# Optimization experiments

Hardware: AMD Instinct MI355X
Metric: run time of the kernel (lower is better)

The kernel has to match this reference:

```python
import jax
import jax.numpy as jnp
from jax import lax
import numpy as np

B, C, Hsp, Wsp = 16, 256, 64, 64
E, HID = 4, 128          # num_experts, expert_hidden
RH = 128                 # router_hidden
TOP_K = 1
EPS = 1e-9


def setup_inputs() -> dict:
    key = jax.random.key(0)
    ks = jax.random.split(key, 8)
    s = lambda *shape: 1.0 / np.sqrt(shape[-1])
    x = jax.random.normal(ks[0], (B, C, Hsp, Wsp), dtype=jnp.float32)
    # router: Linear(C->RH), Linear(RH->E)
    Wr1 = jax.random.normal(ks[1], (RH, C), dtype=jnp.float32) * s(RH, C)
    br1 = jnp.zeros((RH,), dtype=jnp.float32)
    Wr2 = jax.random.normal(ks[2], (E, RH), dtype=jnp.float32) * s(E, RH)
    br2 = jnp.zeros((E,), dtype=jnp.float32)
    # experts (stacked over E): 1x1 C->HID, 3x3 HID->HID, 1x1 HID->C, all bias-free
    W1 = jax.random.normal(ks[3], (E, HID, C), dtype=jnp.float32) * s(E, HID, C)
    W2 = jax.random.normal(ks[4], (E, HID, HID, 3, 3), dtype=jnp.float32) * (1.0 / np.sqrt(HID * 9))
    W3 = jax.random.normal(ks[5], (E, C, HID), dtype=jnp.float32) * s(E, C, HID)
    return {"x": x, "Wr1": Wr1, "br1": br1, "Wr2": Wr2, "br2": br2,
            "W1": W1, "W2": W2, "W3": W3}


def reference(x, Wr1, br1, Wr2, br2, W1, W2, W3):
    b = x.shape[0]
    # --- router on globally pooled features ---
    pooled = x.mean(axis=(2, 3))                      # [B, C]
    h = jax.nn.relu(pooled @ Wr1.T + br1)             # [B, RH]
    logits = h @ Wr2.T + br2                          # [B, E]
    probs = jax.nn.softmax(logits, axis=1)
    # top-k masking + renormalize (top_k < num_experts)
    vals, idx = lax.top_k(probs, TOP_K)               # [B, k]
    mask = jnp.zeros_like(probs).at[jnp.arange(b)[:, None], idx].set(vals)
    probs = mask / (mask.sum(axis=1, keepdims=True) + EPS)
    # --- run all experts (as in original) ---
    # 1x1 conv C->HID, per expert:  [B, E, HID, H, W]
    y1 = jax.nn.relu(jnp.einsum('bcij,ehc->behij', x, W1))
    # 3x3 grouped conv (one group per expert), HID->HID
    y1m = y1.reshape(b, E * HID, Hsp, Wsp)
    y2 = lax.conv_general_dilated(
        y1m, W2.reshape(E * HID, HID, 3, 3),
        window_strides=(1, 1), padding='SAME',
        feature_group_count=E,
        dimension_numbers=('NCHW', 'OIHW', 'NCHW'))
    y2 = jax.nn.relu(y2).reshape(b, E, HID, Hsp, Wsp)
    # 1x1 conv HID->C fused with routed weighted sum over experts + residual
    out = jnp.einsum('begij,ecg,be->bcij', y2, W3, probs) + x
    return out
```

## Files before the change

### kernel.cpp

```cpp
#include <hip/hip_runtime.h>

typedef unsigned short ushort_t;
typedef unsigned int uint32;
typedef __attribute__((ext_vector_type(8))) short s16x8;
typedef __attribute__((ext_vector_type(4))) float f32x4;

#define BB   16
#define CC   256
#define NPX  4096
#define EE   4
#define HID  128
#define RHH  128
#define PW   66
#define PPX  (66*66)

__device__ __forceinline__ ushort_t f2bf(float f) {
  uint32 x = __float_as_uint(f);
  x += 0x7fffu + ((x >> 16) & 1u);
  return (ushort_t)(x >> 16);
}
__device__ __forceinline__ void g2l16(const void* g, void* l) {
  __builtin_amdgcn_global_load_lds((const __attribute__((address_space(1))) uint32*)g,
                                   (__attribute__((address_space(3))) uint32*)l, 16, 0, 0);
}

__global__ __launch_bounds__(256)
void k_xpose(const float* __restrict__ x, ushort_t* __restrict__ xT,
             float* __restrict__ pooled) {
  int px0 = blockIdx.x * 64, c0 = blockIdx.y * 64, b = blockIdx.z;
  int t = threadIdx.x;
  __shared__ float T[64][65];
  const float* xg = x + (size_t)b * CC * NPX;
  int cr = t >> 4, p4 = (t & 15) * 4;
#pragma unroll
  for (int i = 0; i < 4; ++i) {
    float4 v = *(const float4*)(xg + (size_t)(c0 + cr + i * 16) * NPX + px0 + p4);
    T[cr + i * 16][p4 + 0] = v.x; T[cr + i * 16][p4 + 1] = v.y;
    T[cr + i * 16][p4 + 2] = v.z; T[cr + i * 16][p4 + 3] = v.w;
  }
  __syncthreads();
  {
    int c = t >> 2, q = t & 3;
    float s = 0.f;
#pragma unroll
    for (int k = 0; k < 16; ++k) s += T[c][q * 16 + k];
    s += __shfl_down(s, 1, 64);
    s += __shfl_down(s, 2, 64);
    if (q == 0) atomicAdd(&pooled[b * CC + c0 + c], s);
  }
  int px = t >> 2, cg = (t & 3) * 16;
  uint32 o[8];
#pragma unroll
  for (int u = 0; u < 8; ++u) {
    uint32 lo = f2bf(T[cg + 2 * u][px]);
    uint32 hi = f2bf(T[cg + 2 * u + 1][px]);
    o[u] = lo | (hi << 16);
  }
  ushort_t* dst = xT + ((size_t)b * NPX + px0 + px) * CC + c0 + cg;
  *(uint4*)dst = make_uint4(o[0], o[1], o[2], o[3]);
  *(uint4*)(dst + 8) = make_uint4(o[4], o[5], o[6], o[7]);
}

__global__ __launch_bounds__(256)
void k_prep(const float* __restrict__ W1f, const float* __restrict__ W3f,
            const float* __restrict__ W2f, ushort_t* __restrict__ W1b,
            ushort_t* __restrict__ W3b, ushort_t* __restrict__ W2r,
            ushort_t* __restrict__ y1Tp, float* __restrict__ pooled) {
  int bid = blockIdx.x, t = threadIdx.x;
  if (bid < 256) {
    int i4 = (bid * 256 + t) * 4;
    const float* src; ushort_t* dst; int off;
    if (i4 < EE * HID * CC) { src = W1f; dst = W1b; off = i4; }
    else { src = W3f; dst = W3b; off = i4 - EE * HID * CC; }
    float4 v = *(const float4*)(src + off);
    ushort4 o;
    o.x = f2bf(v.x); o.y = f2bf(v.y); o.z = f2bf(v.z); o.w = f2bf(v.w);
    *(ushort4*)(dst + off) = o;
  } else if (bid < 2560) {
    int i = (bid - 256) * 256 + t;
    int h = i & 127;
    int g = (i >> 7) & 127;
    int et = i >> 14;
    int tap = et % 9;
    int e = et / 9;
    W2r[i] = f2bf(W2f[((((size_t)e * 128 + g) * 128 + h) * 3 + tap / 3) * 3 + tap % 3]);
  } else if (bid < 3080) {
    int p = (bid - 2560) * 8 + (t >> 5);
    int b = p / 260, i = p % 260;
    int row, col;
    if (i < 66)       { row = 0;       col = i; }
    else if (i < 132) { row = 65;      col = i - 66; }
    else if (i < 196) { row = i - 131; col = 0; }
    else              { row = i - 195; col = 65; }
    uint2* dst = (uint2*)(y1Tp + (((size_t)b * PPX + row * PW + col) * HID) + (t & 31) * 4);
    *dst = make_uint2(0u, 0u);
  } else {
#pragma unroll
    for (int i = 0; i < 4; ++i)
      *(float4*)&pooled[t * 16 + i * 4] = make_float4(0.f, 0.f, 0.f, 0.f);
  }
}

__global__ __launch_bounds__(128)
void k_router(const float* __restrict__ pooled, const float* __restrict__ Wr1,
              const float* __restrict__ br1, const float* __restrict__ Wr2,
              const float* __restrict__ br2, int* __restrict__ eidx,
              float* __restrict__ gatew) {
  int b = blockIdx.x, t = threadIdx.x;
  __shared__ float hb[RHH];
  __shared__ float lg[EE];
  float s0 = 0.f;
  const float* pb = pooled + b * CC;
  const float* wr = Wr1 + t * CC;
  for (int c = 0; c < CC; ++c) s0 += pb[c] * wr[c];
  float a = br1[t] + s0 * (1.0f / NPX);
  hb[t] = a > 0.f ? a : 0.f;
  __syncthreads();
  if (t < EE) {
    float s = br2[t];
    const float* w2 = Wr2 + t * RHH;
    for (int r = 0; r < RHH; ++r) s += hb[r] * w2[r];
    lg[t] = s;
  }
  __syncthreads();
  if (t == 0) {
    float m = lg[0]; int mi = 0;
    for (int e = 1; e < EE; ++e) if (lg[e] > m) { m = lg[e]; mi = e; }
    float den = 0.f;
    for (int e = 0; e < EE; ++e) den += expf(lg[e] - m);
    float v = 1.0f / den;
    eidx[b] = mi;
    gatew[b] = v / (v + 1e-9f);
  }
}

#define STAGE64(dstA, srcA_expr, dstB, srcB_expr)                         \
  {                                                                       \
    _Pragma("unroll")                                                     \
    for (int s_ = 0; s_ < 4; ++s_) {                                      \
      int ch_ = wave * 4 + s_;                                            \
      int r = ch_ * 8 + (lane >> 3);                                      \
      int kc = ((lane & 7) ^ (lane >> 3)) * 8;                            \
      g2l16(srcA_expr, &dstA[ch_ * 512]);                                 \
      g2l16(srcB_expr, &dstB[ch_ * 512]);                                 \
    }                                                                     \
  }

#define MFMA64(At_, Bt_)                                                  \
  _Pragma("unroll")                                                       \
  for (int kh = 0; kh < 2; ++kh) {                                        \
    s16x8 af[4], bfr[4];                                                  \
    int cidx = ((kh * 4 + (lane >> 4)) ^ (lane & 7)) * 8;                 \
    _Pragma("unroll")                                                     \
    for (int i = 0; i < 4; ++i)                                           \
      af[i] = *(const s16x8*)&At_[(wm + i * 16 + (lane & 15)) * 64 + cidx]; \
    _Pragma("unroll")                                                     \
    for (int j = 0; j < 4; ++j)                                           \
      bfr[j] = *(const s16x8*)&Bt_[(wn + j * 16 + (lane & 15)) * 64 + cidx]; \
    _Pragma("unroll")                                                     \
    for (int i = 0; i < 4; ++i)                                           \
      _Pragma("unroll")                                                   \
      for (int j = 0; j < 4; ++j)                                         \
        acc[i][j] = __builtin_amdgcn_mfma_f32_16x16x32_bf16(af[i], bfr[j], acc[i][j], 0, 0, 0); \
  }

__global__ __launch_bounds__(256)
void k_conv1(const ushort_t* __restrict__ xT, const ushort_t* __restrict__ W1b,
             const int* __restrict__ eidx, ushort_t* __restrict__ y1Tp) {
  int mt = blockIdx.x, b = blockIdx.y;
  int e = eidx[b];
  int t = threadIdx.x, wave = t >> 6, lane = t & 63;
  int wm = (wave & 1) * 64, wn = (wave >> 1) * 64;
  __shared__ ushort_t At[128 * 64];
  __shared__ ushort_t Bt[128 * 64];
  f32x4 acc[4][4] = {};
  const ushort_t* ab = xT + ((size_t)b * NPX + mt * 128) * CC;
  const ushort_t* w1 = W1b + (size_t)e * HID * CC;

  for (int ks = 0; ks < 4; ++ks) {
    int k0 = ks * 64;
    __syncthreads();
    STAGE64(At, ab + (size_t)r * CC + k0 + kc,
            Bt, w1 + (size_t)r * CC + k0 + kc);
    __syncthreads();
    MFMA64(At, Bt);
  }
  ushort_t* yb = y1Tp + (size_t)b * PPX * HID;
#pragma unroll
  for (int i = 0; i < 4; ++i) {
#pragma unroll
    for (int r = 0; r < 4; ++r) {
      int m = wm + i * 16 + (lane >> 4) * 4 + r;
      int prow = mt * 2 + (m >> 6) + 1;
      int pcol = (m & 63) + 1;
      ushort_t* row = yb + ((size_t)prow * PW + pcol) * HID + wn + (lane & 15);
#pragma unroll
      for (int j = 0; j < 4; ++j) {
        float v = acc[i][j][r];
        row[j * 16] = f2bf(v > 0.f ? v : 0.f);
      }
    }
  }
}

__global__ __launch_bounds__(256)
void k_conv2(const ushort_t* __restrict__ y1Tp, const ushort_t* __restrict__ W2r,
             const int* __restrict__ eidx, ushort_t* __restrict__ y2T) {
  int mt = blockIdx.x, b = blockIdx.y;
  int e = eidx[b];
  int t = threadIdx.x, wave = t >> 6, lane = t & 63;
  int wm = (wave & 1) * 64, wn = (wave >> 1) * 64;
  __shared__ ushort_t At[128 * 64];
  __shared__ ushort_t Bt[128 * 64];
  f32x4 acc[4][4] = {};
  const ushort_t* yb = y1Tp + (size_t)b * PPX * HID;
  const ushort_t* w2e = W2r + (size_t)e * 9 * HID * HID;

  for (int tap = 0; tap < 9; ++tap) {
    int dy = tap / 3 - 1, dx = tap % 3 - 1;
    const ushort_t* w2t = w2e + tap * HID * HID;
#pragma unroll
    for (int ks = 0; ks < 2; ++ks) {
      int k0 = ks * 64;
      __syncthreads();
      STAGE64(At, yb + ((size_t)(mt * 2 + (r >> 6) + 1 + dy) * PW + (r & 63) + 1 + dx) * HID + k0 + kc,
              Bt, w2t + (size_t)r * HID + k0 + kc);
      __syncthreads();
      MFMA64(At, Bt);
    }
  }
  ushort_t* ob = y2T + ((size_t)b * NPX + (size_t)mt * 128) * HID;
#pragma unroll
  for (int i = 0; i < 4; ++i) {
#pragma unroll
    for (int r = 0; r < 4; ++r) {
      int m = wm + i * 16 + (lane >> 4) * 4 + r;
      ushort_t* row = ob + (size_t)m * HID + wn + (lane & 15);
#pragma unroll
      for (int j = 0; j < 4; ++j) {
        float v = acc[i][j][r];
        row[j * 16] = f2bf(v > 0.f ? v : 0.f);
      }
    }
  }
}

__global__ __launch_bounds__(256)
void k_conv3(const ushort_t* __restrict__ y2T, const ushort_t* __restrict__ W3b,
             const float* __restrict__ x, const int* __restrict__ eidx,
             const float* __restrict__ gatew, float* __restrict__ out) {
  int mt = blockIdx.x, nt = blockIdx.y, b = blockIdx.z;
  int e = eidx[b];
  float gw = gatew[b];
  int t = threadIdx.x, wave = t >> 6, lane = t & 63;
  int wm = (wave & 1) * 64, wn = (wave >> 1) * 64;
  __shared__ ushort_t At[128 * 64];
  __shared__ ushort_t Bt[128 * 64];
  __shared__ float Tf[32 * 132];
  f32x4 acc[4][4] = {};
  const ushort_t* yb = y2T + ((size_t)b * NPX + (size_t)mt * 128) * HID;
  const ushort_t* w3 = W3b + ((size_t)e * CC + nt * 128) * HID;

#pragma unroll
  for (int ks = 0; ks < 2; ++ks) {
    int k0 = ks * 64;
    __syncthreads();
    STAGE64(At, yb + (size_t)r * HID + k0 + kc,
            Bt, w3 + (size_t)r * HID + k0 + kc);
    __syncthreads();
    MFMA64(At, Bt);
  }
  for (int jj = 0; jj < 4; ++jj) {
    __syncthreads();
    if ((wn >> 6) == (jj >> 1)) {
      int j0 = (jj & 1) * 2;
#pragma unroll
      for (int jd = 0; jd < 2; ++jd) {
        int cl = jd * 16 + (lane & 15);
#pragma unroll
        for (int i = 0; i < 4; ++i) {
          int pb = wm + i * 16 + (lane >> 4) * 4;
          *(f32x4*)&Tf[cl * 132 + pb] = acc[i][j0 + jd];
        }
      }
    }
    __syncthreads();
#pragma unroll
    for (int it = 0; it < 4; ++it) {
      int idx = it * 256 + t;
      int crow = idx >> 5;
      int p4 = (idx & 31) * 4;
      int c = nt * 128 + jj * 32 + crow;
      int px = mt * 128 + p4;
      size_t base = ((size_t)b * CC + c) * NPX + px;
      f32x4 vv = *(const f32x4*)&Tf[crow * 132 + p4];
      f32x4 xa = *(const f32x4*)(x + base);
      vv = gw * vv + xa;
      __builtin_nontemporal_store(vv, (f32x4*)(out + base));
    }
  }
}

extern "C" void kernel_launch(void* const* d_in, const int* in_sizes, int n_in,
                              void* d_out, int out_size, void* d_ws, size_t ws_size,
                              hipStream_t stream) {
  const float* x   = (const float*)d_in[0];
  const float* Wr1 = (const float*)d_in[1];
  const float* br1 = (const float*)d_in[2];
  const float* Wr2 = (const float*)d_in[3];
  const float* br2 = (const float*)d_in[4];
  const float* W1  = (const float*)d_in[5];
  const float* W2  = (const float*)d_in[6];
  const float* W3  = (const float*)d_in[7];
  float* out = (float*)d_out;

  char* ws = (char*)d_ws;
  int*      eidx   = (int*)ws;
  float*    gatew  = (float*)(ws + 64);
  float*    pooled = (float*)(ws + 256);
  ushort_t* W1b    = (ushort_t*)(ws + 16640);
  ushort_t* W3b    = (ushort_t*)(ws + 278784);
  ushort_t* W2r    = (ushort_t*)(ws + 540928);
  ushort_t* y1Tp   = (ushort_t*)(ws + 1720576);
  ushort_t* y2T    = (ushort_t*)(ws + 19562752);
  ushort_t* xT     = (ushort_t*)d_out;

  k_prep  <<<3081, 256, 0, stream>>>(W1, W3, W2, W1b, W3b, W2r, y1Tp, pooled);
  k_xpose <<<dim3(64, 4, 16), 256, 0, stream>>>(x, xT, pooled);
  k_router<<<16, 128, 0, stream>>>(pooled, Wr1, br1, Wr2, br2, eidx, gatew);
  k_conv1 <<<dim3(32, 16), 256, 0, stream>>>(xT, W1b, eidx, y1Tp);
  k_conv2 <<<dim3(32, 16), 256, 0, stream>>>(y1Tp, W2r, eidx, y2T);
  k_conv3 <<<dim3(32, 2, 16), 256, 0, stream>>>(y2T, W3b, x, eidx, gatew, out);
}
```

Before: 195.6 us.

## Fuse 3x3 and output 1x1 conv kernels; merge prep and transpose launches

Fuses the 3x3 grouped conv and the final 1x1 conv with the gated residual into one kernel. The y2 tile stays in swizzled LDS as bf16 instead of round-tripping through global memory. The prep and transpose kernels become one launch, and per-block partial sums replace atomics and the pooled zeroing. In exchange, conv23 uses more LDS per block and runs only 512 blocks, each doing all 256 output channels, so the final stage has less parallelism and the epilogue is serialized per block.

```diff
diff --git a/kernel.cpp b/kernel.cpp
--- a/kernel.cpp
+++ b/kernel.cpp
@@ -25,50 +25,48 @@
 }
 
 __global__ __launch_bounds__(256)
-void k_xpose(const float* __restrict__ x, ushort_t* __restrict__ xT,
-             float* __restrict__ pooled) {
-  int px0 = blockIdx.x * 64, c0 = blockIdx.y * 64, b = blockIdx.z;
-  int t = threadIdx.x;
-  __shared__ float T[64][65];
-  const float* xg = x + (size_t)b * CC * NPX;
-  int cr = t >> 4, p4 = (t & 15) * 4;
-#pragma unroll
-  for (int i = 0; i < 4; ++i) {
-    float4 v = *(const float4*)(xg + (size_t)(c0 + cr + i * 16) * NPX + px0 + p4);
-    T[cr + i * 16][p4 + 0] = v.x; T[cr + i * 16][p4 + 1] = v.y;
-    T[cr + i * 16][p4 + 2] = v.z; T[cr + i * 16][p4 + 3] = v.w;
-  }
-  __syncthreads();
-  {
-    int c = t >> 2, q = t & 3;
-    float s = 0.f;
-#pragma unroll
-    for (int k = 0; k < 16; ++k) s += T[c][q * 16 + k];
-    s += __shfl_down(s, 1, 64);
-    s += __shfl_down(s, 2, 64);
-    if (q == 0) atomicAdd(&pooled[b * CC + c0 + c], s);
-  }
-  int px = t >> 2, cg = (t & 3) * 16;
-  uint32 o[8];
-#pragma unroll
-  for (int u = 0; u < 8; ++u) {
-    uint32 lo = f2bf(T[cg + 2 * u][px]);
-    uint32 hi = f2bf(T[cg + 2 * u + 1][px]);
-    o[u] = lo | (hi << 16);
-  }
-  ushort_t* dst = xT + ((size_t)b * NPX + px0 + px) * CC + c0 + cg;
-  *(uint4*)dst = make_uint4(o[0], o[1], o[2], o[3]);
-  *(uint4*)(dst + 8) = make_uint4(o[4], o[5], o[6], o[7]);
-}
-
-__global__ __launch_bounds__(256)
-void k_prep(const float* __restrict__ W1f, const float* __restrict__ W3f,
-            const float* __restrict__ W2f, ushort_t* __restrict__ W1b,
-            ushort_t* __restrict__ W3b, ushort_t* __restrict__ W2r,
-            ushort_t* __restrict__ y1Tp, float* __restrict__ pooled) {
+void k_xprep(const float* __restrict__ x, ushort_t* __restrict__ xT,
+             float* __restrict__ part,
+             const float* __restrict__ W1f, const float* __restrict__ W3f,
+             const float* __restrict__ W2f, ushort_t* __restrict__ W1b,
+             ushort_t* __restrict__ W3b, ushort_t* __restrict__ W2r,
+             ushort_t* __restrict__ y1Tp) {
   int bid = blockIdx.x, t = threadIdx.x;
-  if (bid < 256) {
-    int i4 = (bid * 256 + t) * 4;
+  if (bid < 4096) {
+    int pxblk = bid & 63, c0 = ((bid >> 6) & 3) * 64, b = bid >> 8;
+    int px0 = pxblk * 64;
+    __shared__ float T[64][65];
+    const float* xg = x + (size_t)b * CC * NPX;
+    int cr = t >> 4, p4 = (t & 15) * 4;
+#pragma unroll
+    for (int i = 0; i < 4; ++i) {
+      float4 v = *(const float4*)(xg + (size_t)(c0 + cr + i * 16) * NPX + px0 + p4);
+      T[cr + i * 16][p4 + 0] = v.x; T[cr + i * 16][p4 + 1] = v.y;
+      T[cr + i * 16][p4 + 2] = v.z; T[cr + i * 16][p4 + 3] = v.w;
+    }
+    __syncthreads();
+    {
+      int c = t >> 2, q = t & 3;
+      float s = 0.f;
+#pragma unroll
+      for (int k = 0; k < 16; ++k) s += T[c][q * 16 + k];
+      s += __shfl_down(s, 1, 64);
+      s += __shfl_down(s, 2, 64);
+      if (q == 0) part[((size_t)b * CC + c0 + c) * 64 + pxblk] = s;
+    }
+    int px = t >> 2, cg = (t & 3) * 16;
+    uint32 o[8];
+#pragma unroll
+    for (int u = 0; u < 8; ++u) {
+      uint32 lo = f2bf(T[cg + 2 * u][px]);
+      uint32 hi = f2bf(T[cg + 2 * u + 1][px]);
+      o[u] = lo | (hi << 16);
+    }
+    ushort_t* dst = xT + ((size_t)b * NPX + px0 + px) * CC + c0 + cg;
+    *(uint4*)dst = make_uint4(o[0], o[1], o[2], o[3]);
+    *(uint4*)(dst + 8) = make_uint4(o[4], o[5], o[6], o[7]);
+  } else if (bid < 4352) {
+    int i4 = ((bid - 4096) * 256 + t) * 4;
     const float* src; ushort_t* dst; int off;
     if (i4 < EE * HID * CC) { src = W1f; dst = W1b; off = i4; }
     else { src = W3f; dst = W3b; off = i4 - EE * HID * CC; }
@@ -76,16 +74,16 @@
     ushort4 o;
     o.x = f2bf(v.x); o.y = f2bf(v.y); o.z = f2bf(v.z); o.w = f2bf(v.w);
     *(ushort4*)(dst + off) = o;
-  } else if (bid < 2560) {
-    int i = (bid - 256) * 256 + t;
+  } else if (bid < 6656) {
+    int i = (bid - 4352) * 256 + t;
     int h = i & 127;
     int g = (i >> 7) & 127;
     int et = i >> 14;
     int tap = et % 9;
     int e = et / 9;
     W2r[i] = f2bf(W2f[((((size_t)e * 128 + g) * 128 + h) * 3 + tap / 3) * 3 + tap % 3]);
-  } else if (bid < 3080) {
-    int p = (bid - 2560) * 8 + (t >> 5);
+  } else {
+    int p = (bid - 6656) * 8 + (t >> 5);
     int b = p / 260, i = p % 260;
     int row, col;
     if (i < 66)       { row = 0;       col = i; }
@@ -94,25 +92,29 @@
     else              { row = i - 195; col = 65; }
     uint2* dst = (uint2*)(y1Tp + (((size_t)b * PPX + row * PW + col) * HID) + (t & 31) * 4);
     *dst = make_uint2(0u, 0u);
-  } else {
-#pragma unroll
-    for (int i = 0; i < 4; ++i)
-      *(float4*)&pooled[t * 16 + i * 4] = make_float4(0.f, 0.f, 0.f, 0.f);
   }
 }
 
 __global__ __launch_bounds__(128)
-void k_router(const float* __restrict__ pooled, const float* __restrict__ Wr1,
+void k_router(const float* __restrict__ part, const float* __restrict__ Wr1,
               const float* __restrict__ br1, const float* __restrict__ Wr2,
               const float* __restrict__ br2, int* __restrict__ eidx,
               float* __restrict__ gatew) {
   int b = blockIdx.x, t = threadIdx.x;
+  __shared__ float spool[CC];
   __shared__ float hb[RHH];
   __shared__ float lg[EE];
+  for (int cc = t; cc < CC; cc += 128) {
+    const float* pp = part + ((size_t)b * CC + cc) * 64;
+    float s = 0.f;
+#pragma unroll
+    for (int k = 0; k < 64; ++k) s += pp[k];
+    spool[cc] = s;
+  }
+  __syncthreads();
   float s0 = 0.f;
-  const float* pb = pooled + b * CC;
   const float* wr = Wr1 + t * CC;
-  for (int c = 0; c < CC; ++c) s0 += pb[c] * wr[c];
+  for (int c = 0; c < CC; ++c) s0 += spool[c] * wr[c];
   float a = br1[t] + s0 * (1.0f / NPX);
   hb[t] = a > 0.f ? a : 0.f;
   __syncthreads();
@@ -146,7 +148,18 @@
     }                                                                     \
   }
 
-#define MFMA64(At_, Bt_)                                                  \
+#define STAGE64B(dstB, srcB_expr)                                         \
+  {                                                                       \
+    _Pragma("unroll")                                                     \
+    for (int s_ = 0; s_ < 4; ++s_) {                                      \
+      int ch_ = wave * 4 + s_;                                            \
+      int r = ch_ * 8 + (lane >> 3);                                      \
+      int kc = ((lane & 7) ^ (lane >> 3)) * 8;                            \
+      g2l16(srcB_expr, &dstB[ch_ * 512]);                                 \
+    }                                                                     \
+  }
+
+#define MFMA64(At_, Bt_, ACC_)                                            \
   _Pragma("unroll")                                                       \
   for (int kh = 0; kh < 2; ++kh) {                                        \
     s16x8 af[4], bfr[4];                                                  \
@@ -161,7 +174,7 @@
     for (int i = 0; i < 4; ++i)                                           \
       _Pragma("unroll")                                                   \
       for (int j = 0; j < 4; ++j)                                         \
-        acc[i][j] = __builtin_amdgcn_mfma_f32_16x16x32_bf16(af[i], bfr[j], acc[i][j], 0, 0, 0); \
+        ACC_[i][j] = __builtin_amdgcn_mfma_f32_16x16x32_bf16(af[i], bfr[j], ACC_[i][j], 0, 0, 0); \
   }
 
 __global__ __launch_bounds__(256)
@@ -183,7 +196,7 @@
     STAGE64(At, ab + (size_t)r * CC + k0 + kc,
             Bt, w1 + (size_t)r * CC + k0 + kc);
     __syncthreads();
-    MFMA64(At, Bt);
+    MFMA64(At, Bt, acc);
   }
   ushort_t* yb = y1Tp + (size_t)b * PPX * HID;
 #pragma unroll
@@ -203,100 +216,93 @@
   }
 }
 
-__global__ __launch_bounds__(256)
-void k_conv2(const ushort_t* __restrict__ y1Tp, const ushort_t* __restrict__ W2r,
-             const int* __restrict__ eidx, ushort_t* __restrict__ y2T) {
+__global__ __launch_bounds__(256, 2)
+void k_conv23(const ushort_t* __restrict__ y1Tp, const ushort_t* __restrict__ W2r,
+              const ushort_t* __restrict__ W3b, const float* __restrict__ x,
+              const int* __restrict__ eidx, const float* __restrict__ gatew,
+              float* __restrict__ out) {
   int mt = blockIdx.x, b = blockIdx.y;
-  int e = eidx[b];
-  int t = threadIdx.x, wave = t >> 6, lane = t & 63;
-  int wm = (wave & 1) * 64, wn = (wave >> 1) * 64;
-  __shared__ ushort_t At[128 * 64];
-  __shared__ ushort_t Bt[128 * 64];
-  f32x4 acc[4][4] = {};
-  const ushort_t* yb = y1Tp + (size_t)b * PPX * HID;
-  const ushort_t* w2e = W2r + (size_t)e * 9 * HID * HID;
-
-  for (int tap = 0; tap < 9; ++tap) {
-    int dy = tap / 3 - 1, dx = tap % 3 - 1;
-    const ushort_t* w2t = w2e + tap * HID * HID;
-#pragma unroll
-    for (int ks = 0; ks < 2; ++ks) {
-      int k0 = ks * 64;
-      __syncthreads();
-      STAGE64(At, yb + ((size_t)(mt * 2 + (r >> 6) + 1 + dy) * PW + (r & 63) + 1 + dx) * HID + k0 + kc,
-              Bt, w2t + (size_t)r * HID + k0 + kc);
-      __syncthreads();
-      MFMA64(At, Bt);
-    }
-  }
-  ushort_t* ob = y2T + ((size_t)b * NPX + (size_t)mt * 128) * HID;
-#pragma unroll
-  for (int i = 0; i < 4; ++i) {
-#pragma unroll
-    for (int r = 0; r < 4; ++r) {
-      int m = wm + i * 16 + (lane >> 4) * 4 + r;
-      ushort_t* row = ob + (size_t)m * HID + wn + (lane & 15);
-#pragma unroll
-      for (int j = 0; j < 4; ++j) {
-        float v = acc[i][j][r];
-        row[j * 16] = f2bf(v > 0.f ? v : 0.f);
-      }
-    }
-  }
-}
-
-__global__ __launch_bounds__(256)
-void k_conv3(const ushort_t* __restrict__ y2T, const ushort_t* __restrict__ W3b,
-             const float* __restrict__ x, const int* __restrict__ eidx,
-             const float* __restrict__ gatew, float* __restrict__ out) {
-  int mt = blockIdx.x, nt = blockIdx.y, b = blockIdx.z;
   int e = eidx[b];
   float gw = gatew[b];
   int t = threadIdx.x, wave = t >> 6, lane = t & 63;
   int wm = (wave & 1) * 64, wn = (wave >> 1) * 64;
-  __shared__ ushort_t At[128 * 64];
-  __shared__ ushort_t Bt[128 * 64];
-  __shared__ float Tf[32 * 132];
+  __shared__ ushort_t bufA[128 * 64];
+  __shared__ ushort_t bufB[128 * 64];
+  __shared__ ushort_t y2s[2][128 * 64];
+  const ushort_t* yb = y1Tp + (size_t)b * PPX * HID;
+  const ushort_t* w2e = W2r + (size_t)e * 9 * HID * HID;
+
   f32x4 acc[4][4] = {};
-  const ushort_t* yb = y2T + ((size_t)b * NPX + (size_t)mt * 128) * HID;
-  const ushort_t* w3 = W3b + ((size_t)e * CC + nt * 128) * HID;
-
-#pragma unroll
-  for (int ks = 0; ks < 2; ++ks) {
-    int k0 = ks * 64;
-    __syncthreads();
-    STAGE64(At, yb + (size_t)r * HID + k0 + kc,
-            Bt, w3 + (size_t)r * HID + k0 + kc);
-    __syncthreads();
-    MFMA64(At, Bt);
-  }
-  for (int jj = 0; jj < 4; ++jj) {
-    __syncthreads();
-    if ((wn >> 6) == (jj >> 1)) {
-      int j0 = (jj & 1) * 2;
-#pragma unroll
-      for (int jd = 0; jd < 2; ++jd) {
-        int cl = jd * 16 + (lane & 15);
-#pragma unroll
-        for (int i = 0; i < 4; ++i) {
-          int pb = wm + i * 16 + (lane >> 4) * 4;
-          *(f32x4*)&Tf[cl * 132 + pb] = acc[i][j0 + jd];
+  for (int tap = 0; tap < 9; ++tap) {
+    int dy = tap / 3 - 1, dx = tap % 3 - 1;
+    const ushort_t* w2t = w2e + tap * HID * HID;
+#pragma unroll
+    for (int ks = 0; ks < 2; ++ks) {
+      int k0 = ks * 64;
+      __syncthreads();
+      STAGE64(bufA, yb + ((size_t)(mt * 2 + (r >> 6) + 1 + dy) * PW + (r & 63) + 1 + dx) * HID + k0 + kc,
+              bufB, w2t + (size_t)r * HID + k0 + kc);
+      __syncthreads();
+      MFMA64(bufA, bufB, acc);
+    }
+  }
+#pragma unroll
+  for (int i = 0; i < 4; ++i)
+#pragma unroll
+    for (int j = 0; j < 4; ++j)
+#pragma unroll
+      for (int r = 0; r < 4; ++r) {
+        int m = wm + i * 16 + (lane >> 4) * 4 + r;
+        int n = wn + j * 16 + (lane & 15);
+        float v = acc[i][j][r];
+        ushort_t bv = f2bf(v > 0.f ? v : 0.f);
+        int nn = n & 63;
+        ushort_t* buf = (n < 64) ? y2s[0] : y2s[1];
+        buf[m * 64 + ((nn >> 3) ^ (m & 7)) * 8 + (nn & 7)] = bv;
+      }
+  __syncthreads();
+  f32x4 acc3[2][4][4] = {};
+  const ushort_t* w3 = W3b + (size_t)e * CC * HID;
+#pragma unroll
+  for (int h = 0; h < 2; ++h) {
+#pragma unroll
+    for (int ks = 0; ks < 2; ++ks) {
+      ushort_t* bt = (ks == 0) ? bufA : bufB;
+      STAGE64B(bt, w3 + (size_t)(h * 128 + r) * HID + ks * 64 + kc);
+      __syncthreads();
+      MFMA64(y2s[ks], bt, acc3[h]);
+    }
+  }
+  float* Tf = (float*)y2s;
+  for (int h = 0; h < 2; ++h) {
+    for (int jj = 0; jj < 4; ++jj) {
+      __syncthreads();
+      if ((wn >> 6) == (jj >> 1)) {
+        int j0 = (jj & 1) * 2;
+#pragma unroll
+        for (int jd = 0; jd < 2; ++jd) {
+          int cl = jd * 16 + (lane & 15);
+#pragma unroll
+          for (int i = 0; i < 4; ++i) {
+            int pb = wm + i * 16 + (lane >> 4) * 4;
+            *(f32x4*)&Tf[cl * 132 + pb] = acc3[h][i][j0 + jd];
+          }
         }
       }
-    }
-    __syncthreads();
-#pragma unroll
-    for (int it = 0; it < 4; ++it) {
-      int idx = it * 256 + t;
-      int crow = idx >> 5;
-      int p4 = (idx & 31) * 4;
-      int c = nt * 128 + jj * 32 + crow;
-      int px = mt * 128 + p4;
-      size_t base = ((size_t)b * CC + c) * NPX + px;
-      f32x4 vv = *(const f32x4*)&Tf[crow * 132 + p4];
-      f32x4 xa = *(const f32x4*)(x + base);
-      vv = gw * vv + xa;
-      __builtin_nontemporal_store(vv, (f32x4*)(out + base));
+      __syncthreads();
+#pragma unroll
+      for (int it = 0; it < 4; ++it) {
+        int idx = it * 256 + t;
+        int crow = idx >> 5;
+        int p4 = (idx & 31) * 4;
+        int c = h * 128 + jj * 32 + crow;
+        int px = mt * 128 + p4;
+        size_t base = ((size_t)b * CC + c) * NPX + px;
+        f32x4 vv = *(const f32x4*)&Tf[crow * 132 + p4];
+        f32x4 xa = *(const f32x4*)(x + base);
+        vv = gw * vv + xa;
+        __builtin_nontemporal_store(vv, (f32x4*)(out + base));
+      }
     }
   }
 }
@@ -315,20 +321,17 @@
   float* out = (float*)d_out;
 
   char* ws = (char*)d_ws;
-  int*      eidx   = (int*)ws;
-  float*    gatew  = (float*)(ws + 64);
-  float*    pooled = (float*)(ws + 256);
-  ushort_t* W1b    = (ushort_t*)(ws + 16640);
-  ushort_t* W3b    = (ushort_t*)(ws + 278784);
-  ushort_t* W2r    = (ushort_t*)(ws + 540928);
-  ushort_t* y1Tp   = (ushort_t*)(ws + 1720576);
-  ushort_t* y2T    = (ushort_t*)(ws + 19562752);
-  ushort_t* xT     = (ushort_t*)d_out;
-
-  k_prep  <<<3081, 256, 0, stream>>>(W1, W3, W2, W1b, W3b, W2r, y1Tp, pooled);
-  k_xpose <<<dim3(64, 4, 16), 256, 0, stream>>>(x, xT, pooled);
-  k_router<<<16, 128, 0, stream>>>(pooled, Wr1, br1, Wr2, br2, eidx, gatew);
+  int*      eidx  = (int*)ws;
+  float*    gatew = (float*)(ws + 64);
+  float*    part  = (float*)(ws + 256);
+  ushort_t* W1b   = (ushort_t*)(ws + 1048832);
+  ushort_t* W3b   = (ushort_t*)(ws + 1310976);
+  ushort_t* W2r   = (ushort_t*)(ws + 1573120);
+  ushort_t* y1Tp  = (ushort_t*)(ws + 2752768);
+  ushort_t* xT    = (ushort_t*)d_out;
+
+  k_xprep <<<7176, 256, 0, stream>>>(x, xT, part, W1, W3, W2, W1b, W3b, W2r, y1Tp);
+  k_router<<<16, 128, 0, stream>>>(part, Wr1, br1, Wr2, br2, eidx, gatew);
   k_conv1 <<<dim3(32, 16), 256, 0, stream>>>(xT, W1b, eidx, y1Tp);
-  k_conv2 <<<dim3(32, 16), 256, 0, stream>>>(y1Tp, W2r, eidx, y2T);
-  k_conv3 <<<dim3(32, 2, 16), 256, 0, stream>>>(y2T, W3b, x, eidx, gatew, out);
-}
+  k_conv23<<<dim3(32, 16), 256, 0, stream>>>(y1Tp, W2r, W3b, x, eidx, gatew, out);
+}
```

Result: faster. 189.1 us (-3.3%).
